# Optimization experiments

Measured on AMD Instinct MI355X. Metric: run time of the kernel, lower is better.

## Reference

```python
import jax, jax.numpy as jnp
import numpy as np

CHUNK = 6  # SmoothLoss chunk length hard-coded in TotalLoss.forward


def setup_inputs() -> dict:
    key = jax.random.key(0)
    k1, k2, k3, k4, k5 = jax.random.split(key, 5)
    N = 3_000_000   # gru/resnet/y length, divisible by 6
    M = 500_000     # one average per 6-sample chunk
    return {
        "resnet_pred": jax.random.normal(k1, (N,), dtype=jnp.float32),
        "gru_pred": jax.random.normal(k2, (N,), dtype=jnp.float32),
        "average_pred": jax.random.normal(k3, (M,), dtype=jnp.float32),
        "y": jax.random.normal(k4, (N,), dtype=jnp.float32),
        "average_hr": jax.random.normal(k5, (M,), dtype=jnp.float32),
    }


def reference(resnet_pred, gru_pred, average_pred, y, average_hr):
    lambda_val = 100.0
    # L1 losses (mean reduction, as nn.L1Loss default)
    l1_loss = jnp.mean(jnp.abs(resnet_pred - y)) + jnp.mean(jnp.abs(average_pred - average_hr))
    # Smoothness loss: for each chunk of 6, sum_t |x_t - mean(chunk)| / 6, summed over chunks
    x = gru_pred.reshape(-1, CHUNK)                      # [C, 6]
    m = jnp.mean(x, axis=1, keepdims=True)               # [C, 1]
    smooth_loss = jnp.sum(jnp.abs(x - m)) / CHUNK        # scalar
    total_loss = l1_loss + lambda_val * smooth_loss
    return (total_loss, l1_loss, smooth_loss)
```

## Files before the change

### kernel.cpp

```cpp
#include <hip/hip_runtime.h>

#define CHUNK 6

__global__ __launch_bounds__(256) void loss_partial_kernel(
    const float* __restrict__ resnet, const float* __restrict__ gru,
    const float* __restrict__ avgp,   const float* __restrict__ y,
    const float* __restrict__ avgh,
    float* __restrict__ partials, int nb, int C, int M)
{
    int idx = blockIdx.x * blockDim.x + threadIdx.x;
    int Cp = C >> 1;
    int Mp = M >> 1;

    float s_l1a = 0.f, s_l1b = 0.f, s_sm = 0.f;

    if (idx < Cp) {
        const float4* g4 = reinterpret_cast<const float4*>(gru) + 3 * idx;
        float4 ga = g4[0], gb = g4[1], gc = g4[2];
        float mA = (ga.x + ga.y + ga.z + ga.w + gb.x + gb.y) * (1.0f / 6.0f);
        float mB = (gb.z + gb.w + gc.x + gc.y + gc.z + gc.w) * (1.0f / 6.0f);
        s_sm = fabsf(ga.x - mA) + fabsf(ga.y - mA) + fabsf(ga.z - mA) + fabsf(ga.w - mA)
             + fabsf(gb.x - mA) + fabsf(gb.y - mA)
             + fabsf(gb.z - mB) + fabsf(gb.w - mB)
             + fabsf(gc.x - mB) + fabsf(gc.y - mB) + fabsf(gc.z - mB) + fabsf(gc.w - mB);

        const float4* r4 = reinterpret_cast<const float4*>(resnet) + 3 * idx;
        const float4* y4 = reinterpret_cast<const float4*>(y) + 3 * idx;
        float4 ra = r4[0], rb = r4[1], rc = r4[2];
        float4 ya = y4[0], yb = y4[1], yc = y4[2];
        s_l1a = fabsf(ra.x - ya.x) + fabsf(ra.y - ya.y) + fabsf(ra.z - ya.z) + fabsf(ra.w - ya.w)
              + fabsf(rb.x - yb.x) + fabsf(rb.y - yb.y) + fabsf(rb.z - yb.z) + fabsf(rb.w - yb.w)
              + fabsf(rc.x - yc.x) + fabsf(rc.y - yc.y) + fabsf(rc.z - yc.z) + fabsf(rc.w - yc.w);
    } else if ((C & 1) && idx == Cp) {
        int base = CHUNK * (C - 1);
        float x0 = gru[base+0], x1 = gru[base+1], x2 = gru[base+2];
        float x3 = gru[base+3], x4 = gru[base+4], x5 = gru[base+5];
        float m = (x0 + x1 + x2 + x3 + x4 + x5) * (1.0f / 6.0f);
        s_sm = fabsf(x0-m)+fabsf(x1-m)+fabsf(x2-m)+fabsf(x3-m)+fabsf(x4-m)+fabsf(x5-m);
        for (int k = 0; k < CHUNK; ++k)
            s_l1a += fabsf(resnet[base+k] - y[base+k]);
    }

    if (idx < Mp) {
        const float2* ap2 = reinterpret_cast<const float2*>(avgp) + idx;
        const float2* ah2 = reinterpret_cast<const float2*>(avgh) + idx;
        float2 ap = *ap2, ah = *ah2;
        s_l1b = fabsf(ap.x - ah.x) + fabsf(ap.y - ah.y);
    } else if ((M & 1) && idx == Mp) {
        s_l1b = fabsf(avgp[M-1] - avgh[M-1]);
    }

    #pragma unroll
    for (int off = 32; off > 0; off >>= 1) {
        s_l1a += __shfl_down(s_l1a, off, 64);
        s_l1b += __shfl_down(s_l1b, off, 64);
        s_sm  += __shfl_down(s_sm,  off, 64);
    }

    __shared__ float red0[4], red1[4], red2[4];
    int wave = threadIdx.x >> 6;
    int lane = threadIdx.x & 63;
    if (lane == 0) { red0[wave] = s_l1a; red1[wave] = s_l1b; red2[wave] = s_sm; }
    __syncthreads();

    if (threadIdx.x == 0) {
        partials[blockIdx.x]          = red0[0] + red0[1] + red0[2] + red0[3];
        partials[nb + blockIdx.x]     = red1[0] + red1[1] + red1[2] + red1[3];
        partials[2 * nb + blockIdx.x] = red2[0] + red2[1] + red2[2] + red2[3];
    }
}

__global__ __launch_bounds__(1024) void loss_reduce_kernel(
    const float* __restrict__ partials, int nb,
    float* __restrict__ out, int N, int M)
{
    double a = 0.0, b = 0.0, c = 0.0;
    for (int i = threadIdx.x; i < nb; i += blockDim.x) {
        a += (double)partials[i];
        b += (double)partials[nb + i];
        c += (double)partials[2 * nb + i];
    }

    #pragma unroll
    for (int off = 32; off > 0; off >>= 1) {
        a += __shfl_down(a, off, 64);
        b += __shfl_down(b, off, 64);
        c += __shfl_down(c, off, 64);
    }

    __shared__ double ra[16], rb[16], rc[16];
    int wave = threadIdx.x >> 6;
    int lane = threadIdx.x & 63;
    int nwaves = (blockDim.x + 63) >> 6;
    if (lane == 0) { ra[wave] = a; rb[wave] = b; rc[wave] = c; }
    __syncthreads();

    if (threadIdx.x == 0) {
        double sa = 0.0, sb = 0.0, sc = 0.0;
        for (int w = 0; w < nwaves; ++w) { sa += ra[w]; sb += rb[w]; sc += rc[w]; }
        double l1     = sa / (double)N + sb / (double)M;
        double smooth = sc / (double)CHUNK;
        double total  = l1 + 100.0 * smooth;
        out[0] = (float)total;
        out[1] = (float)l1;
        out[2] = (float)smooth;
    }
}

extern "C" void kernel_launch(void* const* d_in, const int* in_sizes, int n_in,
                              void* d_out, int out_size, void* d_ws, size_t ws_size,
                              hipStream_t stream) {
    const float* resnet = (const float*)d_in[0];
    const float* gru    = (const float*)d_in[1];
    const float* avgp   = (const float*)d_in[2];
    const float* y      = (const float*)d_in[3];
    const float* avgh   = (const float*)d_in[4];
    float* out = (float*)d_out;

    int N = in_sizes[0];
    int M = in_sizes[2];
    int C = N / CHUNK;

    int Cp = (C >> 1) + (C & 1);
    int Mp = (M >> 1) + (M & 1);
    int work = (Cp > Mp) ? Cp : Mp;
    int block = 256;
    int nb = (work + block - 1) / block;

    float* partials = (float*)d_ws;

    loss_partial_kernel<<<nb, block, 0, stream>>>(resnet, gru, avgp, y, avgh,
                                                  partials, nb, C, M);
    loss_reduce_kernel<<<1, 1024, 0, stream>>>(partials, nb, out, N, M);
}
```

Before: 16.35 us.

## Fuse final reduction into main kernel via last-block atomic ticket

```diff
diff --git a/kernel.cpp b/kernel.cpp
--- a/kernel.cpp
+++ b/kernel.cpp
@@ -2,11 +2,12 @@
 
 #define CHUNK 6
 
-__global__ __launch_bounds__(256) void loss_partial_kernel(
+__global__ __launch_bounds__(1024) void loss_onepass_kernel(
     const float* __restrict__ resnet, const float* __restrict__ gru,
     const float* __restrict__ avgp,   const float* __restrict__ y,
     const float* __restrict__ avgh,
-    float* __restrict__ partials, int nb, int C, int M)
+    int* __restrict__ ticket, float* __restrict__ partials,
+    int nb, int C, int M, int N, float* __restrict__ out)
 {
     int idx = blockIdx.x * blockDim.x + threadIdx.x;
     int Cp = C >> 1;
@@ -57,53 +58,55 @@
         s_sm  += __shfl_down(s_sm,  off, 64);
     }
 
-    __shared__ float red0[4], red1[4], red2[4];
+    __shared__ float red0[16], red1[16], red2[16];
     int wave = threadIdx.x >> 6;
     int lane = threadIdx.x & 63;
     if (lane == 0) { red0[wave] = s_l1a; red1[wave] = s_l1b; red2[wave] = s_sm; }
     __syncthreads();
 
+    __shared__ bool s_last;
     if (threadIdx.x == 0) {
-        partials[blockIdx.x]          = red0[0] + red0[1] + red0[2] + red0[3];
-        partials[nb + blockIdx.x]     = red1[0] + red1[1] + red1[2] + red1[3];
-        partials[2 * nb + blockIdx.x] = red2[0] + red2[1] + red2[2] + red2[3];
+        float p0 = 0.f, p1 = 0.f, p2 = 0.f;
+        #pragma unroll
+        for (int w = 0; w < 16; ++w) { p0 += red0[w]; p1 += red1[w]; p2 += red2[w]; }
+        __hip_atomic_store(&partials[blockIdx.x],          p0, __ATOMIC_RELAXED, __HIP_MEMORY_SCOPE_AGENT);
+        __hip_atomic_store(&partials[nb + blockIdx.x],     p1, __ATOMIC_RELAXED, __HIP_MEMORY_SCOPE_AGENT);
+        __hip_atomic_store(&partials[2 * nb + blockIdx.x], p2, __ATOMIC_RELAXED, __HIP_MEMORY_SCOPE_AGENT);
+        int old = __hip_atomic_fetch_add(ticket, 1, __ATOMIC_ACQ_REL, __HIP_MEMORY_SCOPE_AGENT);
+        s_last = (old == nb - 1);
     }
-}
-
-__global__ __launch_bounds__(1024) void loss_reduce_kernel(
-    const float* __restrict__ partials, int nb,
-    float* __restrict__ out, int N, int M)
-{
-    double a = 0.0, b = 0.0, c = 0.0;
-    for (int i = threadIdx.x; i < nb; i += blockDim.x) {
-        a += (double)partials[i];
-        b += (double)partials[nb + i];
-        c += (double)partials[2 * nb + i];
-    }
-
-    #pragma unroll
-    for (int off = 32; off > 0; off >>= 1) {
-        a += __shfl_down(a, off, 64);
-        b += __shfl_down(b, off, 64);
-        c += __shfl_down(c, off, 64);
-    }
-
-    __shared__ double ra[16], rb[16], rc[16];
-    int wave = threadIdx.x >> 6;
-    int lane = threadIdx.x & 63;
-    int nwaves = (blockDim.x + 63) >> 6;
-    if (lane == 0) { ra[wave] = a; rb[wave] = b; rc[wave] = c; }
     __syncthreads();
 
-    if (threadIdx.x == 0) {
-        double sa = 0.0, sb = 0.0, sc = 0.0;
-        for (int w = 0; w < nwaves; ++w) { sa += ra[w]; sb += rb[w]; sc += rc[w]; }
-        double l1     = sa / (double)N + sb / (double)M;
-        double smooth = sc / (double)CHUNK;
-        double total  = l1 + 100.0 * smooth;
-        out[0] = (float)total;
-        out[1] = (float)l1;
-        out[2] = (float)smooth;
+    if (s_last) {
+        double a = 0.0, b = 0.0, c = 0.0;
+        for (int i = threadIdx.x; i < nb; i += blockDim.x) {
+            a += (double)__hip_atomic_load(&partials[i],          __ATOMIC_RELAXED, __HIP_MEMORY_SCOPE_AGENT);
+            b += (double)__hip_atomic_load(&partials[nb + i],     __ATOMIC_RELAXED, __HIP_MEMORY_SCOPE_AGENT);
+            c += (double)__hip_atomic_load(&partials[2 * nb + i], __ATOMIC_RELAXED, __HIP_MEMORY_SCOPE_AGENT);
+        }
+
+        #pragma unroll
+        for (int off = 32; off > 0; off >>= 1) {
+            a += __shfl_down(a, off, 64);
+            b += __shfl_down(b, off, 64);
+            c += __shfl_down(c, off, 64);
+        }
+
+        __shared__ double ra[16], rb[16], rc[16];
+        if (lane == 0) { ra[wave] = a; rb[wave] = b; rc[wave] = c; }
+        __syncthreads();
+
+        if (threadIdx.x == 0) {
+            double sa = 0.0, sb = 0.0, sc = 0.0;
+            #pragma unroll
+            for (int w = 0; w < 16; ++w) { sa += ra[w]; sb += rb[w]; sc += rc[w]; }
+            double l1     = sa / (double)N + sb / (double)M;
+            double smooth = sc / (double)CHUNK;
+            double total  = l1 + 100.0 * smooth;
+            out[0] = (float)total;
+            out[1] = (float)l1;
+            out[2] = (float)smooth;
+        }
     }
 }
 
@@ -124,12 +127,13 @@
     int Cp = (C >> 1) + (C & 1);
     int Mp = (M >> 1) + (M & 1);
     int work = (Cp > Mp) ? Cp : Mp;
-    int block = 256;
+    int block = 1024;
     int nb = (work + block - 1) / block;
 
-    float* partials = (float*)d_ws;
+    int*   ticket   = (int*)d_ws;
+    float* partials = (float*)((char*)d_ws + 16);
 
-    loss_partial_kernel<<<nb, block, 0, stream>>>(resnet, gru, avgp, y, avgh,
-                                                  partials, nb, C, M);
-    loss_reduce_kernel<<<1, 1024, 0, stream>>>(partials, nb, out, N, M);
+    hipMemsetAsync(ticket, 0, sizeof(int), stream);
+    loss_onepass_kernel<<<nb, block, 0, stream>>>(resnet, gru, avgp, y, avgh,
+                                                  ticket, partials, nb, C, M, N, out);
 }
```

Measured after the change: 21.83 us. 33.5% more time.
